# Performance work log

Hardware: AMD Instinct MI355X
Metric: run time of the kernel (lower is better)

Reference implementation:

```python
import jax, jax.numpy as jnp
import numpy as np

B, Q, K = 4, 512, 512
QUERY_SIZE = 512
KEY_SIZE = 512
NUM_HIDDENS = 256


def setup_inputs() -> dict:
    key = jax.random.key(0)
    k1, k2, k3, k4, k5 = jax.random.split(key, 5)
    queries = jax.random.normal(k1, (B, Q, 1, QUERY_SIZE), dtype=jnp.float32)
    keys = jax.random.normal(k2, (B, 1, K, KEY_SIZE), dtype=jnp.float32)
    # nn.Linear weights (bias=False); stored as (in, out) for einsum clarity
    W_q = jax.random.normal(k3, (QUERY_SIZE, NUM_HIDDENS), dtype=jnp.float32) * (1.0 / np.sqrt(QUERY_SIZE))
    W_k = jax.random.normal(k4, (KEY_SIZE, NUM_HIDDENS), dtype=jnp.float32) * (1.0 / np.sqrt(KEY_SIZE))
    w_v = jax.random.normal(k5, (NUM_HIDDENS,), dtype=jnp.float32) * (1.0 / np.sqrt(NUM_HIDDENS))
    return {"queries": queries, "keys": keys, "W_q": W_q, "W_k": W_k, "w_v": w_v}


def reference(queries, keys, W_q, W_k, w_v):
    # Project: queries (B,Q,1,Dq) -> (B,Q,1,H); keys (B,1,K,Dk) -> (B,1,K,H)
    q = jnp.einsum('bqod,dh->bqoh', queries, W_q)
    k = jnp.einsum('bokd,dh->bokh', keys, W_k)
    # Broadcast add -> (B,Q,K,H), tanh, reduce hidden via w_v -> (B,Q,K)
    features = jnp.tanh(q + k)
    scores = jnp.einsum('bqkh,h->bqk', features, w_v)
    return scores
```

## Files before the change

### kernel.cpp

```cpp
#include <hip/hip_runtime.h>
#include <hip/hip_bf16.h>

#define HH 256
#define DD 512
#define MM 2048
#define CSCALE 2.8853900817779268f

typedef __bf16 bf16x8 __attribute__((ext_vector_type(8)));
typedef float floatx4 __attribute__((ext_vector_type(4)));

__global__ __launch_bounds__(256) void prep_kernel(
    const float* __restrict__ Wq, const float* __restrict__ Wk,
    const float* __restrict__ wv,
    __bf16* __restrict__ Wt, float* __restrict__ wv2, float* __restrict__ sumWp)
{
  const int bx = blockIdx.x;
  if (bx < 256) {
    const int mat  = bx >> 7;
    const int tile = bx & 127;
    const int kt = tile & 15;
    const int nt = tile >> 4;
    const float* __restrict__ W = mat ? Wk : Wq;
    __bf16* __restrict__ Wo = Wt + (size_t)mat * HH * DD;
    __shared__ float lds[32][33];
    const int i = threadIdx.x >> 5;
    const int j = threadIdx.x & 31;
    const int k0 = kt * 32, n0 = nt * 32;
#pragma unroll
    for (int p = 0; p < 4; ++p)
      lds[i + p * 8][j] = W[(k0 + i + p * 8) * HH + n0 + j];
    __syncthreads();
#pragma unroll
    for (int p = 0; p < 4; ++p) {
      const int n = i + p * 8;
      Wo[(n0 + n) * DD + k0 + j] = (__bf16)(lds[j][n] * CSCALE);
    }
  } else {
    __shared__ float red[256];
    const int t = threadIdx.x;
    float w = wv[t];
    wv2[t] = -2.0f * w;
    red[t] = w;
    __syncthreads();
    for (int s = 128; s > 0; s >>= 1) {
      if (t < s) red[t] += red[t + s];
      __syncthreads();
    }
    if (t == 0) *sumWp = red[0];
  }
}

__global__ __launch_bounds__(256, 4) void proj_kernel(
    const float* __restrict__ queries, const float* __restrict__ keys,
    const __bf16* __restrict__ Wt,
    float* __restrict__ eqp, float* __restrict__ ekf)
{
  const int w    = threadIdx.x >> 6;
  const int lane = threadIdx.x & 63;
  const int quad = lane >> 4;
  const int r    = lane & 15;
  const int tw = w & 1;
  const int ks = w >> 1;
  const bool is_k = (blockIdx.z != 0);
  const float* __restrict__ X  = is_k ? keys : queries;
  const __bf16* __restrict__ Wb = Wt + (is_k ? (size_t)HH * DD : 0);

  const int m0 = blockIdx.x * 32 + tw * 16;
  const int n0 = blockIdx.y * 32;

  floatx4 acc0 = {0.f, 0.f, 0.f, 0.f};
  floatx4 acc1 = {0.f, 0.f, 0.f, 0.f};
  const float*  arow = X + (size_t)(m0 + r) * DD + ks * 256 + quad * 8;
  const __bf16* b0   = Wb + (size_t)(n0 + r) * DD + ks * 256 + quad * 8;
  const __bf16* b1   = b0 + 16 * DD;

#pragma unroll
  for (int kk = 0; kk < 256; kk += 32) {
    float4 a0 = *(const float4*)(arow + kk);
    float4 a1 = *(const float4*)(arow + kk + 4);
    bf16x8 af;
    af[0] = (__bf16)a0.x; af[1] = (__bf16)a0.y;
    af[2] = (__bf16)a0.z; af[3] = (__bf16)a0.w;
    af[4] = (__bf16)a1.x; af[5] = (__bf16)a1.y;
    af[6] = (__bf16)a1.z; af[7] = (__bf16)a1.w;
    bf16x8 bf0 = *(const bf16x8*)(b0 + kk);
    bf16x8 bf1 = *(const bf16x8*)(b1 + kk);
    acc0 = __builtin_amdgcn_mfma_f32_16x16x32_bf16(af, bf0, acc0, 0, 0, 0);
    acc1 = __builtin_amdgcn_mfma_f32_16x16x32_bf16(af, bf1, acc1, 0, 0, 0);
  }

  __shared__ float part[2][64][9];
  if (ks == 1) {
#pragma unroll
    for (int i = 0; i < 4; ++i) {
      part[tw][lane][i]     = acc0[i];
      part[tw][lane][4 + i] = acc1[i];
    }
  }
  __syncthreads();
  if (ks == 0) {
#pragma unroll
    for (int i = 0; i < 4; ++i) {
      acc0[i] += part[tw][lane][i];
      acc1[i] += part[tw][lane][4 + i];
    }
    const int mrow = m0 + quad * 4;
    if (!is_k) {
#pragma unroll
      for (int i = 0; i < 4; ++i) {
        eqp[(size_t)(mrow + i) * HH + n0 + r] =
            __builtin_amdgcn_exp2f(acc0[i]);
        eqp[(size_t)(mrow + i) * HH + n0 + 16 + r] =
            __builtin_amdgcn_exp2f(acc1[i]);
      }
    } else {
      const int na = n0 + r, nb = n0 + 16 + r;
#pragma unroll
      for (int i = 0; i < 4; ++i) {
        const int m = mrow + i;
        ekf[((size_t)(m >> 4) * 64 + (na >> 2)) * 64 + (m & 15) * 4 + (na & 3)] =
            __builtin_amdgcn_exp2f(acc0[i]);
        ekf[((size_t)(m >> 4) * 64 + (nb >> 2)) * 64 + (m & 15) * 4 + (nb & 3)] =
            __builtin_amdgcn_exp2f(acc1[i]);
      }
    }
  }
}

__device__ __forceinline__ float quad_term(
    float4 ek, float4 e, float4 w, float acc)
{
  float u0 = fmaf(e.x, ek.x, 1.0f);
  float u1 = fmaf(e.y, ek.y, 1.0f);
  float u2 = fmaf(e.z, ek.z, 1.0f);
  float u3 = fmaf(e.w, ek.w, 1.0f);
  float p01 = u0 * u1;
  float p23 = u2 * u3;
  float n01 = fmaf(w.y, u0, w.x * u1);
  float n23 = fmaf(w.w, u2, w.z * u3);
  acc = fmaf(n01, __builtin_amdgcn_rcpf(p01), acc);
  acc = fmaf(n23, __builtin_amdgcn_rcpf(p23), acc);
  return acc;
}

__global__ __launch_bounds__(256, 4) void score_kernel(
    const float* __restrict__ eqp, const float4* __restrict__ ekf,
    const float* __restrict__ wv2, const float* __restrict__ sumWp,
    float* __restrict__ out)
{
  const int t  = threadIdx.x;
  const int b  = blockIdx.z;
  const int k  = blockIdx.x * 256 + t;
  const int q0 = blockIdx.y * 4;

  const float* __restrict__ e0p = eqp + (size_t)(b * 512 + q0) * HH;
  const float* __restrict__ e1p = e0p + HH;
  const float* __restrict__ e2p = e0p + 2 * HH;
  const float* __restrict__ e3p = e0p + 3 * HH;

  const int m = b * 512 + k;
  const float4* __restrict__ kp =
      ekf + (size_t)(m >> 4) * 1024 + (m & 15);

  float acc0 = 0.f, acc1 = 0.f, acc2 = 0.f, acc3 = 0.f;

  for (int c = 0; c < 16; ++c) {
    float4 kb[4];
#pragma unroll
    for (int i = 0; i < 4; ++i)
      kb[i] = kp[i * 16];
    kp += 64;
#pragma unroll
    for (int i = 0; i < 4; ++i) {
      const int h4 = c * 16 + i * 4;
      float4 w4 = *(const float4*)(wv2 + h4);
      acc0 = quad_term(kb[i], *(const float4*)(e0p + h4), w4, acc0);
      acc1 = quad_term(kb[i], *(const float4*)(e1p + h4), w4, acc1);
      acc2 = quad_term(kb[i], *(const float4*)(e2p + h4), w4, acc2);
      acc3 = quad_term(kb[i], *(const float4*)(e3p + h4), w4, acc3);
    }
  }

  const float sumW = *sumWp;
  float* obase = out + (size_t)(b * 512 + q0) * 512 + blockIdx.x * 256 + t;
  obase[0]    = sumW + acc0;
  obase[512]  = sumW + acc1;
  obase[1024] = sumW + acc2;
  obase[1536] = sumW + acc3;
}

extern "C" void kernel_launch(void* const* d_in, const int* in_sizes, int n_in,
                              void* d_out, int out_size, void* d_ws, size_t ws_size,
                              hipStream_t stream) {
  (void)in_sizes; (void)n_in; (void)out_size; (void)ws_size;
  const float* queries = (const float*)d_in[0];
  const float* Keys    = (const float*)d_in[1];
  const float* Wq      = (const float*)d_in[2];
  const float* Wk      = (const float*)d_in[3];
  const float* wv      = (const float*)d_in[4];
  float* out = (float*)d_out;

  char* ws = (char*)d_ws;
  __bf16* Wt    = (__bf16*)ws;
  float*  wv2   = (float*)(ws + (512 << 10));
  float*  sumWp = (float*)(ws + (513 << 10));
  float*  eqp   = (float*)(ws + (5ull << 20));
  float*  ekf   = (float*)(ws + (8ull << 20));

  prep_kernel<<<dim3(257), 256, 0, stream>>>(Wq, Wk, wv, Wt, wv2, sumWp);
  proj_kernel<<<dim3(64, 8, 2), 256, 0, stream>>>(queries, Keys, Wt, eqp, ekf);
  score_kernel<<<dim3(2, 128, 4), 256, 0, stream>>>(
      eqp, (const float4*)ekf, wv2, sumWp, out);
}
```

Baseline: 112.2 us.

## Combine eight tanh terms per reciprocal using packed float2 math and permuted hidden layout

```diff
diff --git a/kernel.cpp b/kernel.cpp
--- a/kernel.cpp
+++ b/kernel.cpp
@@ -8,6 +8,11 @@
 
 typedef __bf16 bf16x8 __attribute__((ext_vector_type(8)));
 typedef float floatx4 __attribute__((ext_vector_type(4)));
+typedef float floatx2 __attribute__((ext_vector_type(2)));
+
+__device__ __forceinline__ int hperm(int h) {
+  return (h & ~7) | (((h & 3) << 1) | ((h >> 2) & 1));
+}
 
 __global__ __launch_bounds__(256) void prep_kernel(
     const float* __restrict__ Wq, const float* __restrict__ Wk,
@@ -39,7 +44,7 @@
     __shared__ float red[256];
     const int t = threadIdx.x;
     float w = wv[t];
-    wv2[t] = -2.0f * w;
+    wv2[hperm(t)] = -2.0f * w;
     red[t] = w;
     __syncthreads();
     for (int s = 128; s > 0; s >>= 1) {
@@ -105,46 +110,52 @@
       acc1[i] += part[tw][lane][4 + i];
     }
     const int mrow = m0 + quad * 4;
+    const int sa = hperm(n0 + r), sb = hperm(n0 + 16 + r);
     if (!is_k) {
 #pragma unroll
       for (int i = 0; i < 4; ++i) {
-        eqp[(size_t)(mrow + i) * HH + n0 + r] =
+        eqp[(size_t)(mrow + i) * HH + sa] = __builtin_amdgcn_exp2f(acc0[i]);
+        eqp[(size_t)(mrow + i) * HH + sb] = __builtin_amdgcn_exp2f(acc1[i]);
+      }
+    } else {
+#pragma unroll
+      for (int i = 0; i < 4; ++i) {
+        const int m = mrow + i;
+        ekf[((size_t)(m >> 4) * 64 + (sa >> 2)) * 64 + (m & 15) * 4 + (sa & 3)] =
             __builtin_amdgcn_exp2f(acc0[i]);
-        eqp[(size_t)(mrow + i) * HH + n0 + 16 + r] =
+        ekf[((size_t)(m >> 4) * 64 + (sb >> 2)) * 64 + (m & 15) * 4 + (sb & 3)] =
             __builtin_amdgcn_exp2f(acc1[i]);
       }
-    } else {
-      const int na = n0 + r, nb = n0 + 16 + r;
-#pragma unroll
-      for (int i = 0; i < 4; ++i) {
-        const int m = mrow + i;
-        ekf[((size_t)(m >> 4) * 64 + (na >> 2)) * 64 + (m & 15) * 4 + (na & 3)] =
-            __builtin_amdgcn_exp2f(acc0[i]);
-        ekf[((size_t)(m >> 4) * 64 + (nb >> 2)) * 64 + (m & 15) * 4 + (nb & 3)] =
-            __builtin_amdgcn_exp2f(acc1[i]);
-      }
-    }
-  }
-}
-
-__device__ __forceinline__ float quad_term(
-    float4 ek, float4 e, float4 w, float acc)
-{
-  float u0 = fmaf(e.x, ek.x, 1.0f);
-  float u1 = fmaf(e.y, ek.y, 1.0f);
-  float u2 = fmaf(e.z, ek.z, 1.0f);
-  float u3 = fmaf(e.w, ek.w, 1.0f);
-  float p01 = u0 * u1;
-  float p23 = u2 * u3;
-  float n01 = fmaf(w.y, u0, w.x * u1);
-  float n23 = fmaf(w.w, u2, w.z * u3);
-  acc = fmaf(n01, __builtin_amdgcn_rcpf(p01), acc);
-  acc = fmaf(n23, __builtin_amdgcn_rcpf(p23), acc);
-  return acc;
+    }
+  }
+}
+
+__device__ __forceinline__ float octo_term(
+    floatx4 kA, floatx4 kB, floatx4 eA, floatx4 eB,
+    floatx4 wA, floatx4 wB, float acc)
+{
+  const floatx2 one = {1.0f, 1.0f};
+#define LO2(v) __builtin_shufflevector(v, v, 0, 1)
+#define HI2(v) __builtin_shufflevector(v, v, 2, 3)
+  floatx2 u0 = __builtin_elementwise_fma(LO2(eA), LO2(kA), one);
+  floatx2 u1 = __builtin_elementwise_fma(HI2(eA), HI2(kA), one);
+  floatx2 u2 = __builtin_elementwise_fma(LO2(eB), LO2(kB), one);
+  floatx2 u3 = __builtin_elementwise_fma(HI2(eB), HI2(kB), one);
+  floatx2 p01 = u0 * u1;
+  floatx2 p23 = u2 * u3;
+  floatx2 n01 = __builtin_elementwise_fma(LO2(wA), u1, HI2(wA) * u0);
+  floatx2 n23 = __builtin_elementwise_fma(LO2(wB), u3, HI2(wB) * u2);
+  floatx2 Np  = __builtin_elementwise_fma(n23, p01, n01 * p23);
+  floatx2 Pp  = p01 * p23;
+  float N8 = fmaf(Np.x, Pp.y, Np.y * Pp.x);
+  float P8 = Pp.x * Pp.y;
+  return fmaf(N8, __builtin_amdgcn_rcpf(P8), acc);
+#undef LO2
+#undef HI2
 }
 
 __global__ __launch_bounds__(256, 4) void score_kernel(
-    const float* __restrict__ eqp, const float4* __restrict__ ekf,
+    const float* __restrict__ eqp, const floatx4* __restrict__ ekf,
     const float* __restrict__ wv2, const float* __restrict__ sumWp,
     float* __restrict__ out)
 {
@@ -159,26 +170,33 @@
   const float* __restrict__ e3p = e0p + 3 * HH;
 
   const int m = b * 512 + k;
-  const float4* __restrict__ kp =
+  const floatx4* __restrict__ kp =
       ekf + (size_t)(m >> 4) * 1024 + (m & 15);
 
   float acc0 = 0.f, acc1 = 0.f, acc2 = 0.f, acc3 = 0.f;
 
   for (int c = 0; c < 16; ++c) {
-    float4 kb[4];
-#pragma unroll
-    for (int i = 0; i < 4; ++i)
-      kb[i] = kp[i * 16];
+    floatx4 k0 = kp[0];
+    floatx4 k1 = kp[16];
+    floatx4 k2 = kp[32];
+    floatx4 k3 = kp[48];
     kp += 64;
-#pragma unroll
-    for (int i = 0; i < 4; ++i) {
-      const int h4 = c * 16 + i * 4;
-      float4 w4 = *(const float4*)(wv2 + h4);
-      acc0 = quad_term(kb[i], *(const float4*)(e0p + h4), w4, acc0);
-      acc1 = quad_term(kb[i], *(const float4*)(e1p + h4), w4, acc1);
-      acc2 = quad_term(kb[i], *(const float4*)(e2p + h4), w4, acc2);
-      acc3 = quad_term(kb[i], *(const float4*)(e3p + h4), w4, acc3);
-    }
+    const int h0 = c * 16;
+    floatx4 w0 = *(const floatx4*)(wv2 + h0);
+    floatx4 w1 = *(const floatx4*)(wv2 + h0 + 4);
+    floatx4 w2 = *(const floatx4*)(wv2 + h0 + 8);
+    floatx4 w3 = *(const floatx4*)(wv2 + h0 + 12);
+
+#define ROW(accv, ep)                                                     \
+    accv = octo_term(k0, k1, *(const floatx4*)(ep + h0),                  \
+                     *(const floatx4*)(ep + h0 + 4),  w0, w1, accv);      \
+    accv = octo_term(k2, k3, *(const floatx4*)(ep + h0 + 8),              \
+                     *(const floatx4*)(ep + h0 + 12), w2, w3, accv);
+    ROW(acc0, e0p)
+    ROW(acc1, e1p)
+    ROW(acc2, e2p)
+    ROW(acc3, e3p)
+#undef ROW
   }
 
   const float sumW = *sumWp;
@@ -210,5 +228,5 @@
   prep_kernel<<<dim3(257), 256, 0, stream>>>(Wq, Wk, wv, Wt, wv2, sumWp);
   proj_kernel<<<dim3(64, 8, 2), 256, 0, stream>>>(queries, Keys, Wt, eqp, ekf);
   score_kernel<<<dim3(2, 128, 4), 256, 0, stream>>>(
-      eqp, (const float4*)ekf, wv2, sumWp, out);
-}
+      eqp, (const floatx4*)ekf, wv2, sumWp, out);
+}
```

Measured after the change: 107.6 us. -4.1%, faster.
